# Kernel optimization log

Measured on AMD Instinct MI355X. Metric: run time of the kernel, lower is better.

## Reference

```python
import jax, jax.numpy as jnp
import numpy as np

N = 50000      # num nodes
E = 400000     # num edges
D = 384        # input_dim
H = 4          # heads
C = 128        # hidden_dim per head
HC = H * C     # 512


def setup_inputs() -> dict:
    key = jax.random.key(0)
    ks = jax.random.split(key, 32)
    w = lambda k, shape: jax.random.normal(k, shape, jnp.float32) * 0.05
    inp = {
        "x": jax.random.normal(ks[0], (N, D), jnp.float32),
        "edge_index": jax.random.randint(ks[1], (2, E), 0, N, dtype=jnp.int32),
    }
    dims = [(D, HC), (HC, HC)]  # layer0 in=384, layer1 in=512
    i = 2
    for l, (din, dout) in enumerate(dims):
        for nm in ["q", "k", "v", "s"]:  # query/key/value/skip linears
            inp[f"{nm}{l}_w"] = w(ks[i], (dout, din)); i += 1
            inp[f"{nm}{l}_b"] = jnp.zeros((dout,), jnp.float32)
    inp["out_w"] = w(ks[i], (D, HC))
    inp["out_b"] = jnp.zeros((D,), jnp.float32)
    return inp


def _transformer_conv(x, src, dst, Wq, bq, Wk, bk, Wv, bv, Ws, bs):
    # PyG TransformerConv, concat=True, root_weight=True, no edge features.
    n = x.shape[0]
    q = (x @ Wq.T + bq).reshape(n, H, C)
    k = (x @ Wk.T + bk).reshape(n, H, C)
    v = (x @ Wv.T + bv).reshape(n, H, C)
    # per-edge attention logits [E, H]; target = dst, source = src
    alpha = (q[dst] * k[src]).sum(-1) / jnp.sqrt(jnp.float32(C))
    m = jax.ops.segment_max(alpha, dst, num_segments=n)
    m = jnp.where(jnp.isfinite(m), m, 0.0)  # nodes with no in-edges
    e = jnp.exp(alpha - m[dst])
    denom = jax.ops.segment_sum(e, dst, num_segments=n)
    a = e / (denom[dst] + 1e-16)             # segment softmax [E, H]
    msg = v[src] * a[:, :, None]             # [E, H, C]
    agg = jax.ops.segment_sum(msg, dst, num_segments=n).reshape(n, HC)
    return agg + x @ Ws.T + bs               # + root/skip connection


def reference(x, edge_index,
              q0_w, q0_b, k0_w, k0_b, v0_w, v0_b, s0_w, s0_b,
              q1_w, q1_b, k1_w, k1_b, v1_w, v1_b, s1_w, s1_b,
              out_w, out_b):
    src, dst = edge_index[0], edge_index[1]
    h = _transformer_conv(x, src, dst, q0_w, q0_b, k0_w, k0_b, v0_w, v0_b, s0_w, s0_b)
    h = jax.nn.relu(h)
    h = _transformer_conv(h, src, dst, q1_w, q1_b, k1_w, k1_b, v1_w, v1_b, s1_w, s1_b)
    h = jax.nn.relu(h)
    return h @ out_w.T + out_b  # [N, D]
```

## Files before the change

kernel.cpp:

```cpp
#include <hip/hip_runtime.h>
#include <hip/hip_bf16.h>

#define NN 50000
#define NE 400000
#define DD 384
#define HC 512

typedef unsigned int u32;
typedef unsigned short u16;
typedef __attribute__((ext_vector_type(8))) short bf16x8;
typedef __attribute__((ext_vector_type(4))) float f32x4;

#define AS1 __attribute__((address_space(1)))
#define AS3 __attribute__((address_space(3)))

__device__ __forceinline__ float bflo(u32 u){ return __uint_as_float(u << 16); }
__device__ __forceinline__ float bfhi(u32 u){ return __uint_as_float(u & 0xFFFF0000u); }
__device__ __forceinline__ u16 f2bf(float f){
    u32 u = __float_as_uint(f);
    return (u16)((u + 0x7FFFu + ((u >> 16) & 1u)) >> 16);
}
__device__ __forceinline__ u32 pack2(float a, float b){
    return (u32)f2bf(a) | ((u32)f2bf(b) << 16);
}

template<int K>
__global__ __launch_bounds__(512)
void gemm_ws(const u16* __restrict__ Ab, const u16* __restrict__ Wb,
             const float* __restrict__ bias,
             u16* __restrict__ oQ, u16* __restrict__ oK,
             u16* __restrict__ oV, u16* __restrict__ oS)
{
    constexpr int NKT  = K / 64;
    constexpr int WCH  = K / 8;
    constexpr int NPAN = (NN + 127) / 128;
    __shared__ char smW[128 * K * 2];
    __shared__ char smA[2][16384];

    const int b   = blockIdx.x;
    const int xcd = b & 7;
    const int idx = b >> 3;
    const int ct  = idx & 15;
    const int rh  = idx >> 4;

    const int tid  = threadIdx.x;
    const int lane = tid & 63;
    const int w    = tid >> 6;
    const int wq   = w >> 1;
    const int wc   = w & 1;
    const int r16  = lane & 15;
    const int kq   = lane >> 4;

    const u16* Wrow0 = Wb + (size_t)ct * 128 * K;
    #pragma unroll
    for (int p = 0; p < (128 * WCH) / 512; ++p) {
        int ci = p * 512 + tid;
        int row = ci / WCH, pc = ci % WCH;
        int lc = (pc & ~7) | ((pc ^ row) & 7);
        __builtin_amdgcn_global_load_lds((const AS1 u32*)(Wrow0 + (size_t)row * K + lc * 8),
                                         (AS3 u32*)(smW + (size_t)ci * 16), 16, 0, 0);
    }

    auto panel = [&](int j) { return (2 * j + rh) * 8 + xcd; };
    int np = 0;
    while (panel(np) < NPAN) ++np;
    const int total = np * NKT;

    auto stageA = [&](int t) {
        int j = t / NKT, kc = t - (t / NKT) * NKT;
        int m0 = panel(j) * 128;
        #pragma unroll
        for (int p = 0; p < 2; ++p) {
            int ci = p * 512 + tid;
            int row = ci >> 3, pc = ci & 7;
            int lc = pc ^ (row & 7);
            int gr = m0 + row; if (gr >= NN) gr = NN - 1;
            __builtin_amdgcn_global_load_lds((const AS1 u32*)(Ab + (size_t)gr * K + kc * 64 + lc * 8),
                                             (AS3 u32*)(smA[t & 1] + ci * 16), 16, 0, 0);
        }
    };

    stageA(0);
    stageA(1);

    f32x4 acc[2][4] = {};

    const int qsel = ct >> 2;
    u16* outp = (qsel == 0) ? oQ : (qsel == 1) ? oK : (qsel == 2) ? oV : oS;
    const int cb = (ct & 3) * 128 + wc * 64;
    float bv4[4];
    #pragma unroll
    for (int ni = 0; ni < 4; ++ni) bv4[ni] = bias[ct * 128 + wc * 64 + ni * 16 + r16];

    for (int t = 0; t < total; ++t) {
        if (t + 1 < total) { asm volatile("s_waitcnt vmcnt(2)" ::: "memory"); }
        else               { asm volatile("s_waitcnt vmcnt(0)" ::: "memory"); }
        __builtin_amdgcn_s_barrier();
        __builtin_amdgcn_sched_barrier(0);

        const int jj = t / NKT;
        const int kt = t - jj * NKT;
        const char* bufA = smA[t & 1];
        #pragma unroll
        for (int kk = 0; kk < 2; ++kk) {
            bf16x8 av[2], bv[4];
            #pragma unroll
            for (int i = 0; i < 2; ++i) {
                int rowA = wq * 32 + i * 16 + r16;
                int c = kk * 4 + kq;
                av[i] = *(const bf16x8*)(bufA + rowA * 128 + ((c ^ (rowA & 7)) << 4));
            }
            #pragma unroll
            for (int i = 0; i < 4; ++i) {
                int rowW = wc * 64 + i * 16 + r16;
                int c = kt * 8 + kk * 4 + kq;
                int pcw = (c & ~7) | ((c ^ rowW) & 7);
                bv[i] = *(const bf16x8*)(smW + (size_t)rowW * (K * 2) + (pcw << 4));
            }
            #pragma unroll
            for (int mi = 0; mi < 2; ++mi)
                #pragma unroll
                for (int ni = 0; ni < 4; ++ni)
                    acc[mi][ni] = __builtin_amdgcn_mfma_f32_16x16x32_bf16(
                        av[mi], bv[ni], acc[mi][ni], 0, 0, 0);
        }

        __builtin_amdgcn_sched_barrier(0);
        __builtin_amdgcn_s_barrier();
        __builtin_amdgcn_sched_barrier(0);

        if (kt == NKT - 1) {
            int m0 = panel(jj) * 128;
            #pragma unroll
            for (int ni = 0; ni < 4; ++ni) {
                int col = cb + ni * 16 + r16;
                float bb = bv4[ni];
                #pragma unroll
                for (int mi = 0; mi < 2; ++mi)
                    #pragma unroll
                    for (int r = 0; r < 4; ++r) {
                        int gr = m0 + wq * 32 + mi * 16 + kq * 4 + r;
                        if (gr < NN) outp[(size_t)gr * 512 + col] = f2bf(acc[mi][ni][r] + bb);
                        acc[mi][ni][r] = 0.f;
                    }
            }
        }
        if (t + 2 < total) stageA(t + 2);
    }
}

template<int K>
__global__ __launch_bounds__(256)
void gemm2ph(const u16* __restrict__ Ab, const u16* __restrict__ Wb,
             const float* __restrict__ bias, float* __restrict__ oF,
             int n, int Ototal, int NT)
{
    constexpr int NKT = K / 64;
    __shared__ char smA[2][16384];
    __shared__ char smB[2][16384];

    const int nb  = gridDim.x;
    const int bd  = blockIdx.x;
    const int q8  = nb >> 3, r8 = nb & 7;
    const int xcd = bd & 7, gg = bd >> 3;
    const int tt  = (xcd < r8 ? xcd * (q8 + 1) : r8 * (q8 + 1) + (xcd - r8) * q8) + gg;
    const int m0  = (tt / NT) * 128;
    const int o0  = (tt % NT) * 128;

    const int tid  = threadIdx.x;
    const int lane = tid & 63;
    const int w    = tid >> 6;
    const int wr   = w >> 1, wc = w & 1;
    const int r16  = lane & 15;
    const int kq   = lane >> 4;
    const int swz  = (r16 & 7) << 4;

    auto stage = [&](int bf, int kt) {
        #pragma unroll
        for (int p = 0; p < 4; ++p) {
            int ci = p * 256 + tid, row = ci >> 3, pc = ci & 7;
            int lc = pc ^ (row & 7);
            const u16* g = Wb + (size_t)(o0 + row) * K + kt * 64 + lc * 8;
            __builtin_amdgcn_global_load_lds((const AS1 u32*)g,
                                             (AS3 u32*)(smB[bf] + ci * 16), 16, 0, 0);
        }
        #pragma unroll
        for (int p = 0; p < 4; ++p) {
            int ci = p * 256 + tid, row = ci >> 3, pc = ci & 7;
            int lc = pc ^ (row & 7);
            int gr = m0 + row; if (gr >= n) gr = n - 1;
            const u16* g = Ab + (size_t)gr * K + kt * 64 + lc * 8;
            __builtin_amdgcn_global_load_lds((const AS1 u32*)g,
                                             (AS3 u32*)(smA[bf] + ci * 16), 16, 0, 0);
        }
    };

    f32x4 acc[4][4] = {};

    stage(0, 0);
    stage(1, 1);

    for (int kt = 0; kt < NKT; ++kt) {
        if (kt + 1 < NKT) { asm volatile("s_waitcnt vmcnt(8)" ::: "memory"); }
        else             { asm volatile("s_waitcnt vmcnt(0)" ::: "memory"); }
        __builtin_amdgcn_s_barrier();
        __builtin_amdgcn_sched_barrier(0);

        const char* pa = smA[kt & 1] + (wr * 64) * 128;
        const char* pb = smB[kt & 1] + (wc * 64) * 128;
        #pragma unroll
        for (int kk = 0; kk < 2; ++kk) {
            const int kb = kk * 64 + kq * 16;
            bf16x8 av[4], bv[4];
            #pragma unroll
            for (int i = 0; i < 4; ++i) {
                av[i] = *(const bf16x8*)(pa + (i * 16 + r16) * 128 + (kb ^ swz));
                bv[i] = *(const bf16x8*)(pb + (i * 16 + r16) * 128 + (kb ^ swz));
            }
            #pragma unroll
            for (int mi = 0; mi < 4; ++mi)
                #pragma unroll
                for (int ni = 0; ni < 4; ++ni)
                    acc[mi][ni] = __builtin_amdgcn_mfma_f32_16x16x32_bf16(
                        av[mi], bv[ni], acc[mi][ni], 0, 0, 0);
        }

        __builtin_amdgcn_sched_barrier(0);
        __builtin_amdgcn_s_barrier();
        __builtin_amdgcn_sched_barrier(0);
        if (kt + 2 < NKT) stage(kt & 1, kt + 2);
    }

    const int cb = o0 + wc * 64;
    #pragma unroll
    for (int ni = 0; ni < 4; ++ni) {
        int col = cb + ni * 16 + r16;
        float bb = bias[col];
        #pragma unroll
        for (int mi = 0; mi < 4; ++mi)
            #pragma unroll
            for (int r = 0; r < 4; ++r) {
                int gr = m0 + wr * 64 + mi * 16 + kq * 4 + r;
                if (gr < n) oF[(size_t)gr * Ototal + col] = acc[mi][ni][r] + bb;
            }
    }
}

__global__ __launch_bounds__(256)
void cvt_w(const float* __restrict__ src, u16* __restrict__ dst, int n8)
{
    int i = blockIdx.x * 256 + threadIdx.x;
    if (i >= n8) return;
    const float4* s = (const float4*)src + (size_t)i * 2;
    float4 f0 = s[0], f1 = s[1];
    uint4 o;
    o.x = pack2(f0.x, f0.y); o.y = pack2(f0.z, f0.w);
    o.z = pack2(f1.x, f1.y); o.w = pack2(f1.z, f1.w);
    ((uint4*)dst)[i] = o;
}

__global__ __launch_bounds__(256)
void pack_bias(const float* q0, const float* k0, const float* v0, const float* s0,
               const float* q1, const float* k1, const float* v1, const float* s1,
               const float* ob, float* __restrict__ dst)
{
    int i = blockIdx.x * 256 + threadIdx.x;
    if (i >= 4480) return;
    float v;
    if (i < 2048) {
        int j = i & 511, q = i >> 9;
        v = (q == 0 ? q0 : q == 1 ? k0 : q == 2 ? v0 : s0)[j];
    } else if (i < 4096) {
        int j = i - 2048; int q = j >> 9; j &= 511;
        v = (q == 0 ? q1 : q == 1 ? k1 : q == 2 ? v1 : s1)[j];
    } else {
        v = ob[i - 4096];
    }
    dst[i] = v;
}

__global__ __launch_bounds__(256)
void zero_deg(int* __restrict__ deg)
{
    int i = blockIdx.x * 256 + threadIdx.x;
    if (i < NN) deg[i] = 0;
}

__global__ __launch_bounds__(256)
void hist_dst(const int* __restrict__ dst, int* __restrict__ deg)
{
    int e = blockIdx.x * 256 + threadIdx.x;
    if (e < NE) atomicAdd(&deg[dst[e]], 1);
}

__global__ __launch_bounds__(1024)
void scan_deg(const int* __restrict__ deg, int* __restrict__ rowptr,
              int* __restrict__ cursor)
{
    __shared__ int buf[1024];
    __shared__ int carry;
    int tid = threadIdx.x;
    if (tid == 0) carry = 0;
    __syncthreads();
    for (int base = 0; base < NN; base += 1024) {
        int i = base + tid;
        int v = (i < NN) ? deg[i] : 0;
        buf[tid] = v;
        __syncthreads();
        #pragma unroll
        for (int off = 1; off < 1024; off <<= 1) {
            int t = (tid >= off) ? buf[tid - off] : 0;
            __syncthreads();
            buf[tid] += t;
            __syncthreads();
        }
        int excl = carry + buf[tid] - v;
        if (i < NN) { rowptr[i] = excl; cursor[i] = excl; }
        __syncthreads();
        if (tid == 0) carry += buf[1023];
        __syncthreads();
    }
    if (tid == 0) rowptr[NN] = NE;
}

__global__ __launch_bounds__(256)
void scatter_edges(const int* __restrict__ src, const int* __restrict__ dst,
                   int* __restrict__ cursor, int* __restrict__ esrc_ord)
{
    int e = blockIdx.x * 256 + threadIdx.x;
    if (e >= NE) return;
    int pos = atomicAdd(&cursor[dst[e]], 1);
    esrc_ord[pos] = src[e];
}

__global__ __launch_bounds__(256)
void node_attn(const u16* __restrict__ Qb, const u16* __restrict__ Kb,
               const u16* __restrict__ Vb, const int* __restrict__ rowptr,
               const int* __restrict__ esrc, const u16* __restrict__ skipb,
               u16* __restrict__ outb)
{
    int d = blockIdx.x * 4 + (threadIdx.x >> 6);
    if (d >= NN) return;
    int lane = threadIdx.x & 63;

    uint4 qv = *((const uint4*)(Qb + (size_t)d * HC) + lane);
    float q[8] = { bflo(qv.x), bfhi(qv.x), bflo(qv.y), bfhi(qv.y),
                   bflo(qv.z), bfhi(qv.z), bflo(qv.w), bfhi(qv.w) };

    int beg = rowptr[d], end = rowptr[d + 1];
    float m = -INFINITY, den = 0.f;
    float acc[8] = {};

    for (int i = beg; i < end; ++i) {
        int s = esrc[i];
        uint4 kv = *((const uint4*)(Kb + (size_t)s * HC) + lane);
        float sum = q[0] * bflo(kv.x) + q[1] * bfhi(kv.x)
                  + q[2] * bflo(kv.y) + q[3] * bfhi(kv.y)
                  + q[4] * bflo(kv.z) + q[5] * bfhi(kv.z)
                  + q[6] * bflo(kv.w) + q[7] * bfhi(kv.w);
        #pragma unroll
        for (int off = 1; off < 16; off <<= 1) sum += __shfl_xor(sum, off, 64);
        float alpha = sum * 0.08838834764831845f;

        float mnew  = fmaxf(m, alpha);
        float scale = __expf(m - mnew);
        float p     = __expf(alpha - mnew);
        den = den * scale + p;

        uint4 vv = *((const uint4*)(Vb + (size_t)s * HC) + lane);
        acc[0] = acc[0] * scale + p * bflo(vv.x);
        acc[1] = acc[1] * scale + p * bfhi(vv.x);
        acc[2] = acc[2] * scale + p * bflo(vv.y);
        acc[3] = acc[3] * scale + p * bfhi(vv.y);
        acc[4] = acc[4] * scale + p * bflo(vv.z);
        acc[5] = acc[5] * scale + p * bfhi(vv.z);
        acc[6] = acc[6] * scale + p * bflo(vv.w);
        acc[7] = acc[7] * scale + p * bfhi(vv.w);
        m = mnew;
    }

    float inv = 1.f / (den + 1e-16f);
    size_t base = (size_t)d * HC + lane * 8;
    uint4 sv = *((const uint4*)(skipb + base));
    float sk[8] = { bflo(sv.x), bfhi(sv.x), bflo(sv.y), bfhi(sv.y),
                    bflo(sv.z), bfhi(sv.z), bflo(sv.w), bfhi(sv.w) };
    uint4 o;
    o.x = pack2(fmaxf(acc[0] * inv + sk[0], 0.f), fmaxf(acc[1] * inv + sk[1], 0.f));
    o.y = pack2(fmaxf(acc[2] * inv + sk[2], 0.f), fmaxf(acc[3] * inv + sk[3], 0.f));
    o.z = pack2(fmaxf(acc[4] * inv + sk[4], 0.f), fmaxf(acc[5] * inv + sk[5], 0.f));
    o.w = pack2(fmaxf(acc[6] * inv + sk[6], 0.f), fmaxf(acc[7] * inv + sk[7], 0.f));
    *(uint4*)(outb + base) = o;
}

extern "C" void kernel_launch(void* const* d_in, const int* in_sizes, int n_in,
                              void* d_out, int out_size, void* d_ws, size_t ws_size,
                              hipStream_t stream)
{
    const float* x   = (const float*)d_in[0];
    const int* ei    = (const int*)d_in[1];
    const int* esrc  = ei;
    const int* edst  = ei + NE;
    const float* q0w = (const float*)d_in[2];  const float* q0b = (const float*)d_in[3];
    const float* k0w = (const float*)d_in[4];  const float* k0b = (const float*)d_in[5];
    const float* v0w = (const float*)d_in[6];  const float* v0b = (const float*)d_in[7];
    const float* s0w = (const float*)d_in[8];  const float* s0b = (const float*)d_in[9];
    const float* q1w = (const float*)d_in[10]; const float* q1b = (const float*)d_in[11];
    const float* k1w = (const float*)d_in[12]; const float* k1b = (const float*)d_in[13];
    const float* v1w = (const float*)d_in[14]; const float* v1b = (const float*)d_in[15];
    const float* s1w = (const float*)d_in[16]; const float* s1b = (const float*)d_in[17];
    const float* ow  = (const float*)d_in[18]; const float* obs = (const float*)d_in[19];

    char* p = (char*)d_ws;
    auto take = [&](size_t bytes) { void* r = (void*)p; p += (bytes + 255) & ~(size_t)255; return r; };
    u16*   Qb     = (u16*)take((size_t)NN * HC * 2);
    u16*   Vb     = (u16*)take((size_t)NN * HC * 2);
    u16*   Hb     = (u16*)take((size_t)NN * HC * 2);
    u16*   Sb     = (u16*)take((size_t)NN * HC * 2);
    u16*   Xb     = (u16*)take((size_t)NN * DD * 2);
    u16*   Wc0    = (u16*)take((size_t)2048 * DD * 2);
    u16*   Wc1    = (u16*)take((size_t)2048 * HC * 2);
    u16*   WcO    = (u16*)take((size_t)DD * HC * 2);
    float* barena = (float*)take(4480 * 4);

    char* dob = (char*)d_out;
    u16* Kb       = (u16*)dob;
    int* deg      = (int*)(dob + 51200000);
    int* rowptr   = (int*)(dob + 51400192);
    int* cursor   = (int*)(dob + 51600384);
    int* esrc_ord = (int*)(dob + 51800576);

    dim3 blk(256);
    int gN   = (NN + 255) / 256;
    int gE   = (NE + 255) / 256;
    int gnod = (NN + 3) / 4;
    const int NPAN = (NN + 127) / 128;
    int go = NPAN * 3;

    pack_bias<<<(4480 + 255) / 256, blk, 0, stream>>>(q0b, k0b, v0b, s0b,
                                                      q1b, k1b, v1b, s1b, obs, barena);
    const int xn8 = NN * DD / 8;
    const int w0n8 = 512 * DD / 8, w1n8 = 512 * HC / 8, won8 = DD * HC / 8;
    cvt_w<<<(xn8 + 255) / 256, blk, 0, stream>>>(x, Xb, xn8);
    cvt_w<<<(w0n8 + 255) / 256, blk, 0, stream>>>(q0w, Wc0 + 0 * 512 * DD, w0n8);
    cvt_w<<<(w0n8 + 255) / 256, blk, 0, stream>>>(k0w, Wc0 + 1 * 512 * DD, w0n8);
    cvt_w<<<(w0n8 + 255) / 256, blk, 0, stream>>>(v0w, Wc0 + 2 * 512 * DD, w0n8);
    cvt_w<<<(w0n8 + 255) / 256, blk, 0, stream>>>(s0w, Wc0 + 3 * 512 * DD, w0n8);
    cvt_w<<<(w1n8 + 255) / 256, blk, 0, stream>>>(q1w, Wc1 + 0 * 512 * HC, w1n8);
    cvt_w<<<(w1n8 + 255) / 256, blk, 0, stream>>>(k1w, Wc1 + 1 * 512 * HC, w1n8);
    cvt_w<<<(w1n8 + 255) / 256, blk, 0, stream>>>(v1w, Wc1 + 2 * 512 * HC, w1n8);
    cvt_w<<<(w1n8 + 255) / 256, blk, 0, stream>>>(s1w, Wc1 + 3 * 512 * HC, w1n8);
    cvt_w<<<(won8 + 255) / 256, blk, 0, stream>>>(ow, WcO, won8);

    zero_deg      <<<gN, blk, 0, stream>>>(deg);
    hist_dst      <<<gE, blk, 0, stream>>>(edst, deg);
    scan_deg      <<<1, 1024, 0, stream>>>(deg, rowptr, cursor);
    scatter_edges <<<gE, blk, 0, stream>>>(esrc, edst, cursor, esrc_ord);

    gemm_ws<DD><<<256, 512, 0, stream>>>(Xb, Wc0, barena, Qb, Kb, Vb, Sb);
    node_attn<<<gnod, blk, 0, stream>>>(Qb, Kb, Vb, rowptr, esrc_ord, Sb, Hb);

    gemm_ws<HC><<<256, 512, 0, stream>>>(Hb, Wc1, barena + 2048, Qb, Kb, Vb, Sb);
    node_attn<<<gnod, blk, 0, stream>>>(Qb, Kb, Vb, rowptr, esrc_ord, Sb, Hb);

    gemm2ph<HC><<<go, blk, 0, stream>>>(Hb, WcO, barena + 4096,
                                        (float*)d_out, NN, 384, 3);
}
```

Measured before the change: 777.0 us.

## Restructure weight-stationary GEMM k-tiling, fuse conversion kernels, use wave-shuffle scan

The weight-stationary QKVS GEMM now stages A in 32-wide k chunks covering two row panels per stage, so each B fragment read from LDS feeds twice as many MFMAs. Weights are loaded into a k-chunk-major swizzled LDS layout through ordinary loads instead of direct-to-LDS loads. The ten separate fp32-to-bf16 conversion launches are merged into one kernel, and the degree prefix scan uses wave shuffles instead of a barrier-heavy LDS Hillis-Steele scan. The cost is more accumulator registers and a different pipeline depth per byte staged.

```diff
diff --git a/kernel.cpp b/kernel.cpp
--- a/kernel.cpp
+++ b/kernel.cpp
@@ -31,10 +31,9 @@
              u16* __restrict__ oQ, u16* __restrict__ oK,
              u16* __restrict__ oV, u16* __restrict__ oS)
 {
-    constexpr int NKT  = K / 64;
-    constexpr int WCH  = K / 8;
+    constexpr int NKC  = K / 32;
     constexpr int NPAN = (NN + 127) / 128;
-    __shared__ char smW[128 * K * 2];
+    __shared__ char smW[NKC * 8192];
     __shared__ char smA[2][16384];
 
     const int b   = blockIdx.x;
@@ -51,39 +50,44 @@
     const int r16  = lane & 15;
     const int kq   = lane >> 4;
 
-    const u16* Wrow0 = Wb + (size_t)ct * 128 * K;
-    #pragma unroll
-    for (int p = 0; p < (128 * WCH) / 512; ++p) {
-        int ci = p * 512 + tid;
-        int row = ci / WCH, pc = ci % WCH;
-        int lc = (pc & ~7) | ((pc ^ row) & 7);
-        __builtin_amdgcn_global_load_lds((const AS1 u32*)(Wrow0 + (size_t)row * K + lc * 8),
-                                         (AS3 u32*)(smW + (size_t)ci * 16), 16, 0, 0);
-    }
-
-    auto panel = [&](int j) { return (2 * j + rh) * 8 + xcd; };
+    {
+        const u16* Wrow0 = Wb + (size_t)ct * 128 * K;
+        const int row = tid >> 2, pc = tid & 3;
+        const int lc  = pc ^ (row & 3);
+        #pragma unroll
+        for (int kt = 0; kt < NKC; ++kt) {
+            uint4 v = *(const uint4*)(Wrow0 + (size_t)row * K + kt * 32 + lc * 8);
+            *(uint4*)(smW + kt * 8192 + tid * 16) = v;
+        }
+    }
+    asm volatile("s_waitcnt lgkmcnt(0)" ::: "memory");
+    __builtin_amdgcn_sched_barrier(0);
+
     int np = 0;
-    while (panel(np) < NPAN) ++np;
-    const int total = np * NKT;
-
-    auto stageA = [&](int t) {
-        int j = t / NKT, kc = t - (t / NKT) * NKT;
-        int m0 = panel(j) * 128;
+    while ((2 * np + rh) * 8 + xcd < NPAN) ++np;
+    const int npair = (np + 1) / 2;
+    const int total = npair * NKC;
+
+    auto stageA = [&](int t2) {
+        int jp2 = t2 / NKC, kc2 = t2 - jp2 * NKC;
+        int p0 = (4 * jp2 + rh) * 8 + xcd;
+        int p1 = (2 * jp2 + 1 < np) ? p0 + 16 : p0;
+        const int row = tid >> 2, pc = tid & 3;
+        const int lc  = pc ^ (row & 3);
         #pragma unroll
         for (int p = 0; p < 2; ++p) {
-            int ci = p * 512 + tid;
-            int row = ci >> 3, pc = ci & 7;
-            int lc = pc ^ (row & 7);
-            int gr = m0 + row; if (gr >= NN) gr = NN - 1;
-            __builtin_amdgcn_global_load_lds((const AS1 u32*)(Ab + (size_t)gr * K + kc * 64 + lc * 8),
-                                             (AS3 u32*)(smA[t & 1] + ci * 16), 16, 0, 0);
+            int pan = p ? p1 : p0;
+            int gr = pan * 128 + row; if (gr >= NN) gr = NN - 1;
+            __builtin_amdgcn_global_load_lds(
+                (const AS1 u32*)(Ab + (size_t)gr * K + kc2 * 32 + lc * 8),
+                (AS3 u32*)(smA[t2 & 1] + (p * 512 + tid) * 16), 16, 0, 0);
         }
     };
 
     stageA(0);
-    stageA(1);
-
-    f32x4 acc[2][4] = {};
+    if (total > 1) stageA(1);
+
+    f32x4 acc[2][2][4] = {};
 
     const int qsel = ct >> 2;
     u16* outp = (qsel == 0) ? oQ : (qsel == 1) ? oK : (qsel == 2) ? oV : oS;
@@ -98,51 +102,55 @@
         __builtin_amdgcn_s_barrier();
         __builtin_amdgcn_sched_barrier(0);
 
-        const int jj = t / NKT;
-        const int kt = t - jj * NKT;
+        const int jp = t / NKC;
+        const int kc = t - jp * NKC;
         const char* bufA = smA[t & 1];
-        #pragma unroll
-        for (int kk = 0; kk < 2; ++kk) {
-            bf16x8 av[2], bv[4];
-            #pragma unroll
-            for (int i = 0; i < 2; ++i) {
-                int rowA = wq * 32 + i * 16 + r16;
-                int c = kk * 4 + kq;
-                av[i] = *(const bf16x8*)(bufA + rowA * 128 + ((c ^ (rowA & 7)) << 4));
-            }
-            #pragma unroll
-            for (int i = 0; i < 4; ++i) {
-                int rowW = wc * 64 + i * 16 + r16;
-                int c = kt * 8 + kk * 4 + kq;
-                int pcw = (c & ~7) | ((c ^ rowW) & 7);
-                bv[i] = *(const bf16x8*)(smW + (size_t)rowW * (K * 2) + (pcw << 4));
-            }
-            #pragma unroll
-            for (int mi = 0; mi < 2; ++mi)
+
+        bf16x8 bv[4];
+        #pragma unroll
+        for (int ni = 0; ni < 4; ++ni) {
+            int rowW = wc * 64 + ni * 16 + r16;
+            bv[ni] = *(const bf16x8*)(smW + kc * 8192 + rowW * 64
+                                      + ((kq ^ (rowW & 3)) << 4));
+        }
+        #pragma unroll
+        for (int q = 0; q < 2; ++q) {
+            #pragma unroll
+            for (int mi = 0; mi < 2; ++mi) {
+                int rowA = wq * 32 + mi * 16 + r16;
+                bf16x8 av = *(const bf16x8*)(bufA + q * 8192 + rowA * 64
+                                             + ((kq ^ (rowA & 3)) << 4));
                 #pragma unroll
                 for (int ni = 0; ni < 4; ++ni)
-                    acc[mi][ni] = __builtin_amdgcn_mfma_f32_16x16x32_bf16(
-                        av[mi], bv[ni], acc[mi][ni], 0, 0, 0);
+                    acc[q][mi][ni] = __builtin_amdgcn_mfma_f32_16x16x32_bf16(
+                        av, bv[ni], acc[q][mi][ni], 0, 0, 0);
+            }
         }
 
         __builtin_amdgcn_sched_barrier(0);
         __builtin_amdgcn_s_barrier();
         __builtin_amdgcn_sched_barrier(0);
 
-        if (kt == NKT - 1) {
-            int m0 = panel(jj) * 128;
-            #pragma unroll
-            for (int ni = 0; ni < 4; ++ni) {
-                int col = cb + ni * 16 + r16;
-                float bb = bv4[ni];
+        if (kc == NKC - 1) {
+            int p0 = (4 * jp + rh) * 8 + xcd;
+            int p1 = (2 * jp + 1 < np) ? p0 + 16 : p0;
+            #pragma unroll
+            for (int q = 0; q < 2; ++q) {
+                int m0 = (q ? p1 : p0) * 128;
                 #pragma unroll
-                for (int mi = 0; mi < 2; ++mi)
+                for (int ni = 0; ni < 4; ++ni) {
+                    int col = cb + ni * 16 + r16;
+                    float bb = bv4[ni];
                     #pragma unroll
-                    for (int r = 0; r < 4; ++r) {
-                        int gr = m0 + wq * 32 + mi * 16 + kq * 4 + r;
-                        if (gr < NN) outp[(size_t)gr * 512 + col] = f2bf(acc[mi][ni][r] + bb);
-                        acc[mi][ni][r] = 0.f;
-                    }
+                    for (int mi = 0; mi < 2; ++mi)
+                        #pragma unroll
+                        for (int r = 0; r < 4; ++r) {
+                            int gr = m0 + wq * 32 + mi * 16 + kq * 4 + r;
+                            if (gr < NN)
+                                outp[(size_t)gr * 512 + col] = f2bf(acc[q][mi][ni][r] + bb);
+                            acc[q][mi][ni][r] = 0.f;
+                        }
+                }
             }
         }
         if (t + 2 < total) stageA(t + 2);
@@ -231,10 +239,10 @@
         if (kt + 2 < NKT) stage(kt & 1, kt + 2);
     }
 
-    const int cb = o0 + wc * 64;
+    const int cbo = o0 + wc * 64;
     #pragma unroll
     for (int ni = 0; ni < 4; ++ni) {
-        int col = cb + ni * 16 + r16;
+        int col = cbo + ni * 16 + r16;
         float bb = bias[col];
         #pragma unroll
         for (int mi = 0; mi < 4; ++mi)
@@ -246,17 +254,42 @@
     }
 }
 
-__global__ __launch_bounds__(256)
-void cvt_w(const float* __restrict__ src, u16* __restrict__ dst, int n8)
+#define XG  2400000
+#define W0G 24576
+#define W1G 32768
+#define WOG 24576
+#define CVT_TOTAL (XG + 4*W0G + 4*W1G + WOG)
+
+__global__ __launch_bounds__(256)
+void cvt_all(const float* __restrict__ x,
+             const float* q0w, const float* k0w, const float* v0w, const float* s0w,
+             const float* q1w, const float* k1w, const float* v1w, const float* s1w,
+             const float* ow,
+             u16* __restrict__ Xb, u16* __restrict__ Wc0,
+             u16* __restrict__ Wc1, u16* __restrict__ WcO)
 {
     int i = blockIdx.x * 256 + threadIdx.x;
-    if (i >= n8) return;
-    const float4* s = (const float4*)src + (size_t)i * 2;
-    float4 f0 = s[0], f1 = s[1];
+    if (i >= CVT_TOTAL) return;
+    const float* s; u16* d; int g;
+    if (i < XG) { s = x; d = Xb; g = i; }
+    else {
+        int j = i - XG;
+        if (j < 4 * W0G) {
+            int q = j / W0G; g = j - q * W0G;
+            s = (q == 0 ? q0w : q == 1 ? k0w : q == 2 ? v0w : s0w);
+            d = Wc0 + (size_t)q * W0G * 8;
+        } else if ((j -= 4 * W0G) < 4 * W1G) {
+            int q = j / W1G; g = j - q * W1G;
+            s = (q == 0 ? q1w : q == 1 ? k1w : q == 2 ? v1w : s1w);
+            d = Wc1 + (size_t)q * W1G * 8;
+        } else { j -= 4 * W1G; s = ow; d = WcO; g = j; }
+    }
+    float4 f0 = ((const float4*)s)[(size_t)g * 2];
+    float4 f1 = ((const float4*)s)[(size_t)g * 2 + 1];
     uint4 o;
     o.x = pack2(f0.x, f0.y); o.y = pack2(f0.z, f0.w);
     o.z = pack2(f1.x, f1.y); o.w = pack2(f1.z, f1.w);
-    ((uint4*)dst)[i] = o;
+    ((uint4*)d)[g] = o;
 }
 
 __global__ __launch_bounds__(256)
@@ -297,27 +330,35 @@
 void scan_deg(const int* __restrict__ deg, int* __restrict__ rowptr,
               int* __restrict__ cursor)
 {
-    __shared__ int buf[1024];
-    __shared__ int carry;
-    int tid = threadIdx.x;
-    if (tid == 0) carry = 0;
-    __syncthreads();
+    __shared__ int wsum[16];
+    const int tid = threadIdx.x, lane = tid & 63, wid = tid >> 6;
+    int carry = 0;
     for (int base = 0; base < NN; base += 1024) {
         int i = base + tid;
-        int v = (i < NN) ? deg[i] : 0;
-        buf[tid] = v;
+        int orig = (i < NN) ? deg[i] : 0;
+        int v = orig;
+        #pragma unroll
+        for (int off = 1; off < 64; off <<= 1) {
+            int t = __shfl_up(v, off, 64);
+            if (lane >= off) v += t;
+        }
+        if (lane == 63) wsum[wid] = v;
         __syncthreads();
-        #pragma unroll
-        for (int off = 1; off < 1024; off <<= 1) {
-            int t = (tid >= off) ? buf[tid - off] : 0;
-            __syncthreads();
-            buf[tid] += t;
-            __syncthreads();
-        }
-        int excl = carry + buf[tid] - v;
+        if (wid == 0) {
+            int s = (lane < 16) ? wsum[lane] : 0;
+            #pragma unroll
+            for (int off = 1; off < 16; off <<= 1) {
+                int t = __shfl_up(s, off, 16);
+                if ((lane & 15) >= off) s += t;
+            }
+            if (lane < 16) wsum[lane] = s;
+        }
+        __syncthreads();
+        int woff  = (wid == 0) ? 0 : wsum[wid - 1];
+        int total = wsum[15];
+        int excl  = carry + woff + (v - orig);
         if (i < NN) { rowptr[i] = excl; cursor[i] = excl; }
-        __syncthreads();
-        if (tid == 0) carry += buf[1023];
+        carry += total;
         __syncthreads();
     }
     if (tid == 0) rowptr[NN] = NE;
@@ -438,18 +479,8 @@
 
     pack_bias<<<(4480 + 255) / 256, blk, 0, stream>>>(q0b, k0b, v0b, s0b,
                                                       q1b, k1b, v1b, s1b, obs, barena);
-    const int xn8 = NN * DD / 8;
-    const int w0n8 = 512 * DD / 8, w1n8 = 512 * HC / 8, won8 = DD * HC / 8;
-    cvt_w<<<(xn8 + 255) / 256, blk, 0, stream>>>(x, Xb, xn8);
-    cvt_w<<<(w0n8 + 255) / 256, blk, 0, stream>>>(q0w, Wc0 + 0 * 512 * DD, w0n8);
-    cvt_w<<<(w0n8 + 255) / 256, blk, 0, stream>>>(k0w, Wc0 + 1 * 512 * DD, w0n8);
-    cvt_w<<<(w0n8 + 255) / 256, blk, 0, stream>>>(v0w, Wc0 + 2 * 512 * DD, w0n8);
-    cvt_w<<<(w0n8 + 255) / 256, blk, 0, stream>>>(s0w, Wc0 + 3 * 512 * DD, w0n8);
-    cvt_w<<<(w1n8 + 255) / 256, blk, 0, stream>>>(q1w, Wc1 + 0 * 512 * HC, w1n8);
-    cvt_w<<<(w1n8 + 255) / 256, blk, 0, stream>>>(k1w, Wc1 + 1 * 512 * HC, w1n8);
-    cvt_w<<<(w1n8 + 255) / 256, blk, 0, stream>>>(v1w, Wc1 + 2 * 512 * HC, w1n8);
-    cvt_w<<<(w1n8 + 255) / 256, blk, 0, stream>>>(s1w, Wc1 + 3 * 512 * HC, w1n8);
-    cvt_w<<<(won8 + 255) / 256, blk, 0, stream>>>(ow, WcO, won8);
+    cvt_all<<<(CVT_TOTAL + 255) / 256, blk, 0, stream>>>(x,
+        q0w, k0w, v0w, s0w, q1w, k1w, v1w, s1w, ow, Xb, Wc0, Wc1, WcO);
 
     zero_deg      <<<gN, blk, 0, stream>>>(deg);
     hist_dst      <<<gE, blk, 0, stream>>>(edst, deg);
```

Result: faster. 736.3 us (-5.2%).
